# Optimization experiments

Hardware: AMD Instinct MI355X
Metric: run time of the kernel (lower is better)

Reference implementation:

```python
import jax, jax.numpy as jnp
import numpy as np

B, S, H, MAX_LEN = 32, 1024, 384, 8192


def setup_inputs() -> dict:
    key = jax.random.key(0)
    k0, k1, k2 = jax.random.split(key, 3)
    x = jax.random.normal(k0, (B, S, H), dtype=jnp.float32)
    src_mask = jnp.ones((B, S), dtype=bool)
    mel_mask = jnp.ones((B, MAX_LEN), dtype=bool)
    duration_target = jax.random.randint(k1, (B, S), 0, 8)
    pitch_target = jax.random.normal(k2, (B, MAX_LEN), dtype=jnp.float32)
    return {
        "x": x,
        "src_mask": src_mask,
        "mel_mask": mel_mask,
        "duration_target": duration_target,
        "pitch_target": pitch_target,
        "max_len": MAX_LEN,
    }


def _length_regulate(x, duration, max_len):
    """Vectorized repeat_interleave + pad.

    Frame t of batch b copies source vector j where
    cumsum(duration)[b, j-1] <= t < cumsum(duration)[b, j].
    """
    cum = jnp.cumsum(duration, axis=1)                      # [B, S]
    mel_len = cum[:, -1]                                    # [B]
    t = jnp.arange(max_len)                                 # [MAX]
    # searchsorted(side='right') maps frame index -> source index
    idx = jax.vmap(lambda c: jnp.searchsorted(c, t, side="right"))(cum)  # [B, MAX]
    idx = jnp.minimum(idx, x.shape[1] - 1)
    out = jnp.take_along_axis(x, idx[:, :, None], axis=1)   # [B, MAX, H]
    valid = t[None, :] < mel_len[:, None]                   # [B, MAX]  (zero padding)
    out = jnp.where(valid[:, :, None], out, jnp.zeros((), out.dtype))
    return out, mel_len


def reference(x, src_mask, mel_mask, duration_target, pitch_target, max_len):
    out, mel_len = _length_regulate(x, duration_target, max_len)
    return (out, mel_len, mel_mask)
```

## Files before the change

### kernel.cpp

```cpp
#include <hip/hip_runtime.h>

#define BB 32
#define SS 1024
#define HH 384
#define MAXLEN 8192
#define H4 (HH / 4)
#define OUT0 (BB * MAXLEN * HH)
#define MEL_OFF OUT0
#define MASK_OFF (OUT0 + BB)

typedef float vfloat4 __attribute__((ext_vector_type(4)));

__global__ __launch_bounds__(1024) void k_prep(
    const int* __restrict__ dur,
    const int* __restrict__ mel_mask_in,
    float* __restrict__ out,
    int* __restrict__ idxbuf)
{
    __shared__ int cum[SS];
    const int b = blockIdx.x;
    const int tid = threadIdx.x;

    cum[tid] = dur[b * SS + tid];
    for (int off = 1; off < SS; off <<= 1) {
        __syncthreads();
        int v = (tid >= off) ? cum[tid - off] : 0;
        __syncthreads();
        cum[tid] += v;
    }
    __syncthreads();

    const int mel_len = cum[SS - 1];
    if (tid == 0) out[MEL_OFF + b] = (float)mel_len;

    for (int k = 0; k < MAXLEN / SS; ++k) {
        const int t = tid + k * SS;
        int lo = 0, hi = SS;
        while (lo < hi) {
            int mid = (lo + hi) >> 1;
            if (cum[mid] <= t) lo = mid + 1; else hi = mid;
        }
        int idx = (lo < SS) ? lo : (SS - 1);
        idxbuf[b * MAXLEN + t] = (t < mel_len) ? idx : -1;
        out[MASK_OFF + b * MAXLEN + t] = mel_mask_in[b * MAXLEN + t] ? 1.0f : 0.0f;
    }
}

#define FPB 16
#define ITEMS 6
#define NB_EXP (BB * MAXLEN / FPB)
__global__ __launch_bounds__(256) void k_expand(
    const vfloat4* __restrict__ x4,
    const int* __restrict__ idxbuf,
    vfloat4* __restrict__ out4)
{
    __shared__ int sidx[FPB];
    const int L = blockIdx.x;
    const int W = (L & 7) * (NB_EXP / 8) + (L >> 3);
    const int f0 = W * FPB;
    if (threadIdx.x < FPB) sidx[threadIdx.x] = idxbuf[f0 + threadIdx.x];
    __syncthreads();

    const int b = f0 >> 13;
    const size_t xb = (size_t)b * SS * H4;
    const size_t ob = (size_t)f0 * H4;
#pragma unroll
    for (int k = 0; k < ITEMS; ++k) {
        const int j = (int)threadIdx.x + k * 256;
        const int fl = j / H4;
        const int c  = j - fl * H4;
        const int id = sidx[fl];
        vfloat4 v = (vfloat4)(0.f);
        if (id >= 0) v = x4[xb + (size_t)id * H4 + c];
        __builtin_nontemporal_store(v, &out4[ob + j]);
    }
}

extern "C" void kernel_launch(void* const* d_in, const int* in_sizes, int n_in,
                              void* d_out, int out_size, void* d_ws, size_t ws_size,
                              hipStream_t stream) {
    const float* x = (const float*)d_in[0];
    const int* mel_mask_in = (const int*)d_in[2];
    const int* dur = (const int*)d_in[3];
    float* out = (float*)d_out;
    int* idxbuf = (int*)d_ws;

    k_prep<<<BB, 1024, 0, stream>>>(dur, mel_mask_in, out, idxbuf);
    k_expand<<<NB_EXP, 256, 0, stream>>>((const vfloat4*)x, idxbuf, (vfloat4*)out);
}
```

Measured before the change: 446.9 us.

## Fuse prefix-sum and index search into expand kernel, drop prep kernel

Removes the separate prep kernel. Each expand block now recomputes the full 1024-element cumulative sum of its batch row, using a wave-shuffle scan over int4 loads, then binary-searches only its own 16 frames directly into shared memory. This removes one kernel launch, the idxbuf round trip through global memory and the serialization between the two kernels. In exchange, every one of the 16384 blocks redundantly reads 4 KB of durations and runs a scan before it can start copying.

```diff
diff --git a/kernel.cpp b/kernel.cpp
--- a/kernel.cpp
+++ b/kernel.cpp
@@ -11,68 +11,79 @@
 
 typedef float vfloat4 __attribute__((ext_vector_type(4)));
 
-__global__ __launch_bounds__(1024) void k_prep(
+#define FPB 16
+#define ITEMS 6
+#define NB_EXP (BB * MAXLEN / FPB)
+__global__ __launch_bounds__(256) void k_fused(
+    const vfloat4* __restrict__ x4,
     const int* __restrict__ dur,
     const int* __restrict__ mel_mask_in,
-    float* __restrict__ out,
-    int* __restrict__ idxbuf)
+    float* __restrict__ out)
 {
     __shared__ int cum[SS];
-    const int b = blockIdx.x;
+    __shared__ int wsum[4];
+    __shared__ int sidx[FPB];
+
+    const int L = blockIdx.x;
+    const int W = (L & 7) * (NB_EXP / 8) + (L >> 3);
+    const int f0 = W * FPB;
+    const int b  = f0 >> 13;
+    const int t0 = f0 & (MAXLEN - 1);
     const int tid = threadIdx.x;
+    const int lane = tid & 63;
+    const int wid = tid >> 6;
 
-    cum[tid] = dur[b * SS + tid];
-    for (int off = 1; off < SS; off <<= 1) {
-        __syncthreads();
-        int v = (tid >= off) ? cum[tid - off] : 0;
-        __syncthreads();
-        cum[tid] += v;
+    const int4 d4 = ((const int4*)dur)[b * (SS / 4) + tid];
+    const int l0 = d4.x;
+    const int l1 = l0 + d4.y;
+    const int l2 = l1 + d4.z;
+    const int l3 = l2 + d4.w;
+    int v = l3;
+#pragma unroll
+    for (int o = 1; o < 64; o <<= 1) {
+        int u = __shfl_up(v, o, 64);
+        if (lane >= o) v += u;
     }
+    if (lane == 63) wsum[wid] = v;
+    __syncthreads();
+    int woff = 0;
+#pragma unroll
+    for (int w = 0; w < 3; ++w) woff += (wid > w) ? wsum[w] : 0;
+    const int excl = woff + v - l3;
+    cum[4 * tid + 0] = excl + l0;
+    cum[4 * tid + 1] = excl + l1;
+    cum[4 * tid + 2] = excl + l2;
+    cum[4 * tid + 3] = excl + l3;
     __syncthreads();
 
     const int mel_len = cum[SS - 1];
-    if (tid == 0) out[MEL_OFF + b] = (float)mel_len;
+    if (t0 == 0 && tid == 0) out[MEL_OFF + b] = (float)mel_len;
 
-    for (int k = 0; k < MAXLEN / SS; ++k) {
-        const int t = tid + k * SS;
+    if (tid < FPB) {
+        const int t = t0 + tid;
         int lo = 0, hi = SS;
         while (lo < hi) {
             int mid = (lo + hi) >> 1;
             if (cum[mid] <= t) lo = mid + 1; else hi = mid;
         }
         int idx = (lo < SS) ? lo : (SS - 1);
-        idxbuf[b * MAXLEN + t] = (t < mel_len) ? idx : -1;
+        sidx[tid] = (t < mel_len) ? idx : -1;
         out[MASK_OFF + b * MAXLEN + t] = mel_mask_in[b * MAXLEN + t] ? 1.0f : 0.0f;
     }
-}
-
-#define FPB 16
-#define ITEMS 6
-#define NB_EXP (BB * MAXLEN / FPB)
-__global__ __launch_bounds__(256) void k_expand(
-    const vfloat4* __restrict__ x4,
-    const int* __restrict__ idxbuf,
-    vfloat4* __restrict__ out4)
-{
-    __shared__ int sidx[FPB];
-    const int L = blockIdx.x;
-    const int W = (L & 7) * (NB_EXP / 8) + (L >> 3);
-    const int f0 = W * FPB;
-    if (threadIdx.x < FPB) sidx[threadIdx.x] = idxbuf[f0 + threadIdx.x];
     __syncthreads();
 
-    const int b = f0 >> 13;
     const size_t xb = (size_t)b * SS * H4;
     const size_t ob = (size_t)f0 * H4;
+    vfloat4* __restrict__ out4 = (vfloat4*)out;
 #pragma unroll
     for (int k = 0; k < ITEMS; ++k) {
-        const int j = (int)threadIdx.x + k * 256;
+        const int j = tid + k * 256;
         const int fl = j / H4;
         const int c  = j - fl * H4;
         const int id = sidx[fl];
-        vfloat4 v = (vfloat4)(0.f);
-        if (id >= 0) v = x4[xb + (size_t)id * H4 + c];
-        __builtin_nontemporal_store(v, &out4[ob + j]);
+        vfloat4 val = (vfloat4)(0.f);
+        if (id >= 0) val = x4[xb + (size_t)id * H4 + c];
+        __builtin_nontemporal_store(val, &out4[ob + j]);
     }
 }
 
@@ -83,8 +94,6 @@
     const int* mel_mask_in = (const int*)d_in[2];
     const int* dur = (const int*)d_in[3];
     float* out = (float*)d_out;
-    int* idxbuf = (int*)d_ws;
 
-    k_prep<<<BB, 1024, 0, stream>>>(dur, mel_mask_in, out, idxbuf);
-    k_expand<<<NB_EXP, 256, 0, stream>>>((const vfloat4*)x, idxbuf, (vfloat4*)out);
+    k_fused<<<NB_EXP, 256, 0, stream>>>((const vfloat4*)x, dur, mel_mask_in, out);
 }
```

Result: no change. 442.0 us (-1.1%).
